# Kernel tuning notes

Measured on AMD Instinct MI355X. Metric: run time of the kernel, lower is better.

## Reference

```python
import jax, jax.numpy as jnp
from jax import lax
import numpy as np

B, C, H, W = 1, 128, 32, 32
OC, K = 128, 3
STRIDE, PAD, DIL = 1, 1, 1
ARRAY_SIZE = 32
QUANT = 8


def setup_inputs() -> dict:
    key = jax.random.key(0)
    k1, k2, k3 = jax.random.split(key, 3)
    x = jax.random.normal(k1, (B, C, H, W), dtype=jnp.float32)
    weight = jax.random.normal(k2, (OC, C, K, K), dtype=jnp.float32) * 0.05
    bias = jax.random.normal(k3, (OC,), dtype=jnp.float32) * 0.05
    return {"x": x, "weight": weight, "bias": bias}


def _conv(x, w, b):
    out = lax.conv_general_dilated(
        x, w, window_strides=(STRIDE, STRIDE),
        padding=((PAD, PAD), (PAD, PAD)),
        rhs_dilation=(DIL, DIL),
        dimension_numbers=("NCHW", "OIHW", "NCHW"))
    return out + b[None, :, None, None]


def _unfold(x, oh, ow):
    # torch F.unfold: (B, C*K*K, L) with channel-major ordering (c, kh, kw)
    xp = jnp.pad(x, ((0, 0), (0, 0), (PAD, PAD), (PAD, PAD)))
    cols = jnp.stack(
        [xp[:, :, i:i + oh, j:j + ow] for i in range(K) for j in range(K)],
        axis=2)  # (B, C, K*K, OH, OW)
    return cols.reshape(B, C * K * K, oh * ow)


def reference(x, weight, bias):
    oh = (H + 2 * PAD - DIL * (K - 1) - 1) // STRIDE + 1
    ow = (W + 2 * PAD - DIL * (K - 1) - 1) // STRIDE + 1
    L = oh * ow
    qmax = float(2 ** QUANT - 1)

    # --- set_quant_params: per-spatial-location scale/zero_point from full conv out ---
    out_full = _conv(x, weight, bias).reshape(1, OC, -1)  # (1, OC, L)
    mx = jnp.max(out_full, axis=1)  # (1, L)
    mn = jnp.min(out_full, axis=1)
    scale = (mx - mn) / qmax
    zp = jnp.clip(-mn / scale, 0.0, qmax)
    zp = jnp.where(jnp.isnan(zp), 0.0, zp)
    zp = jnp.trunc(zp)  # .int() truncation
    scale = lax.stop_gradient(scale)[:, None, None, :]  # (1,1,1,L)
    zp = lax.stop_gradient(zp)[:, None, None, :]

    # --- unfold + explicit elementwise multiply (crossbar expansion) ---
    cols = _unfold(x, oh, ow)                       # (B, C*K*K, L)
    pre = cols[:, None, :, :] * weight.reshape(1, OC, C * K * K, 1)  # (B,OC,CKK,L)

    # pad front of dim 2 to a multiple of array_size (pads a full chunk if divisible)
    ckk = C * K * K
    pad_d3 = ARRAY_SIZE - ckk % ARRAY_SIZE
    pre = jnp.pad(pre, ((0, 0), (0, 0), (pad_d3, 0), (0, 0)))

    # block-sum over array_size chunks (crossbar partial sums)
    n_chunks = (ckk + pad_d3) // ARRAY_SIZE
    accu = pre.reshape(B, OC, n_chunks, ARRAY_SIZE, L).sum(axis=3)  # (B,OC,n_chunks,L)

    # per-chunk fake-quant (Quant8F) with straight-through estimator
    q = jnp.clip(jnp.round(accu / scale) + zp, 0.0, qmax)
    deq = (q - zp) * scale
    quant_accu = accu + lax.stop_gradient(deq - accu)

    # reduce over chunks -> conv output (note: bias is NOT added in original forward)
    return quant_accu.sum(axis=2).reshape(B, OC, oh, ow)
```

## Files before the change

kernel.cpp:

```cpp
#include <hip/hip_runtime.h>

#define L_     1024
#define CKK_   1152
#define QMAX_  255.0f
#define NCH    36
#define PSTR_  (131072 + 64)

__global__ __launch_bounds__(256) void gemm_chunks(
    const float* __restrict__ x,
    const float* __restrict__ w,
    float* __restrict__ planes)
{
    __shared__ __align__(16) float Wb[32][132];
    __shared__ __align__(16) float xs[32][64];

    const int t   = threadIdx.x;
    const int l0  = blockIdx.x * 64;
    const int j   = blockIdx.y;
    const int d0  = j * 32;
    const int oh0 = l0 >> 5;

    float4 wld[4];
    int    wo[4], wk[4];
#pragma unroll
    for (int it = 0; it < 4; it++) {
        const int f4 = it * 256 + t;
        wo[it]  = f4 >> 3;
        wk[it]  = (f4 & 7) * 4;
        wld[it] = *(const float4*)(w + wo[it] * CKK_ + d0 + wk[it]);
    }

    float xl[8];
    int   xk[8], xll[8];
#pragma unroll
    for (int it = 0; it < 8; it++) {
        const int e  = it * 256 + t;
        const int k  = e >> 6, ll = e & 63;
        const int d  = d0 + k;
        const int c  = d / 9, r = d - 9 * c;
        const int kh = r / 3, kw = r - 3 * kh;
        const int iy = oh0 + (ll >> 5) + kh - 1;
        const int ix = (ll & 31) + kw - 1;
        const bool ok = ((unsigned)iy < 32u) & ((unsigned)ix < 32u);
        const int idx = ok ? (c * 1024 + iy * 32 + ix) : 0;
        const float v = x[idx];
        xl[it] = ok ? v : 0.f;
        xk[it] = k; xll[it] = ll;
    }

#pragma unroll
    for (int it = 0; it < 4; it++) {
        Wb[wk[it] + 0][wo[it]] = wld[it].x;
        Wb[wk[it] + 1][wo[it]] = wld[it].y;
        Wb[wk[it] + 2][wo[it]] = wld[it].z;
        Wb[wk[it] + 3][wo[it]] = wld[it].w;
    }
#pragma unroll
    for (int it = 0; it < 8; it++)
        xs[xk[it]][xll[it]] = xl[it];
    __syncthreads();

    const int oc0 = (t & 31) * 4;
    const int ll0 = (t >> 5) * 8;
    float acc[4][8];
#pragma unroll
    for (int r = 0; r < 4; r++)
#pragma unroll
        for (int i = 0; i < 8; i++) acc[r][i] = 0.f;

#pragma unroll
    for (int k = 0; k < 32; k++) {
        const float4 wv = *(const float4*)&Wb[k][oc0];
        const float4 xa = *(const float4*)&xs[k][ll0];
        const float4 xb = *(const float4*)&xs[k][ll0 + 4];
        acc[0][0] = fmaf(wv.x, xa.x, acc[0][0]);
        acc[0][1] = fmaf(wv.x, xa.y, acc[0][1]);
        acc[0][2] = fmaf(wv.x, xa.z, acc[0][2]);
        acc[0][3] = fmaf(wv.x, xa.w, acc[0][3]);
        acc[0][4] = fmaf(wv.x, xb.x, acc[0][4]);
        acc[0][5] = fmaf(wv.x, xb.y, acc[0][5]);
        acc[0][6] = fmaf(wv.x, xb.z, acc[0][6]);
        acc[0][7] = fmaf(wv.x, xb.w, acc[0][7]);
        acc[1][0] = fmaf(wv.y, xa.x, acc[1][0]);
        acc[1][1] = fmaf(wv.y, xa.y, acc[1][1]);
        acc[1][2] = fmaf(wv.y, xa.z, acc[1][2]);
        acc[1][3] = fmaf(wv.y, xa.w, acc[1][3]);
        acc[1][4] = fmaf(wv.y, xb.x, acc[1][4]);
        acc[1][5] = fmaf(wv.y, xb.y, acc[1][5]);
        acc[1][6] = fmaf(wv.y, xb.z, acc[1][6]);
        acc[1][7] = fmaf(wv.y, xb.w, acc[1][7]);
        acc[2][0] = fmaf(wv.z, xa.x, acc[2][0]);
        acc[2][1] = fmaf(wv.z, xa.y, acc[2][1]);
        acc[2][2] = fmaf(wv.z, xa.z, acc[2][2]);
        acc[2][3] = fmaf(wv.z, xa.w, acc[2][3]);
        acc[2][4] = fmaf(wv.z, xb.x, acc[2][4]);
        acc[2][5] = fmaf(wv.z, xb.y, acc[2][5]);
        acc[2][6] = fmaf(wv.z, xb.z, acc[2][6]);
        acc[2][7] = fmaf(wv.z, xb.w, acc[2][7]);
        acc[3][0] = fmaf(wv.w, xa.x, acc[3][0]);
        acc[3][1] = fmaf(wv.w, xa.y, acc[3][1]);
        acc[3][2] = fmaf(wv.w, xa.z, acc[3][2]);
        acc[3][3] = fmaf(wv.w, xa.w, acc[3][3]);
        acc[3][4] = fmaf(wv.w, xb.x, acc[3][4]);
        acc[3][5] = fmaf(wv.w, xb.y, acc[3][5]);
        acc[3][6] = fmaf(wv.w, xb.z, acc[3][6]);
        acc[3][7] = fmaf(wv.w, xb.w, acc[3][7]);
    }

    float* dst = planes + (size_t)j * PSTR_ + (size_t)l0 * 128;
#pragma unroll
    for (int i = 0; i < 8; i++)
        *(float4*)(dst + (ll0 + i) * 128 + oc0) =
            make_float4(acc[0][i], acc[1][i], acc[2][i], acc[3][i]);
}

__global__ __launch_bounds__(256) void fused_mq(
    const float* __restrict__ planes,
    const float* __restrict__ bias,
    float* __restrict__ out)
{
    __shared__ float part[256];
    __shared__ float mnb[128], mxb[128];
    __shared__ float s_sc, s_zp, s_iv;
    const int t  = threadIdx.x;
    const int oc = t & 127, jh = t >> 7;
    const int l  = blockIdx.x;

    const float* p = planes + (size_t)(jh * 18) * PSTR_ + (size_t)l * 128 + oc;
    float v[18];
#pragma unroll
    for (int j = 0; j < 18; j++) v[j] = p[(size_t)j * PSTR_];

    float s = 0.f;
#pragma unroll
    for (int j = 0; j < 18; j++) s += v[j];
    part[t] = s;
    __syncthreads();

    if (t < 128) {
        const float tot = part[t] + part[t + 128] + bias[t];
        mnb[t] = tot;
        mxb[t] = tot;
    }
    __syncthreads();
#pragma unroll
    for (int st = 64; st > 0; st >>= 1) {
        if (t < st) {
            mnb[t] = fminf(mnb[t], mnb[t + st]);
            mxb[t] = fmaxf(mxb[t], mxb[t + st]);
        }
        __syncthreads();
    }
    if (t == 0) {
        const float amn = mnb[0], amx = mxb[0];
        const float sv  = (amx - amn) / QMAX_;
        float z = -amn / sv;
        z = fmaxf(z, 0.f);
        z = fminf(z, QMAX_);
        z = truncf(z);
        s_sc = sv;
        s_zp = z;
        s_iv = 1.0f / sv;
    }
    __syncthreads();

    const float sc = s_sc, zv = s_zp, iv = s_iv;
    float q = 0.f;
#pragma unroll
    for (int j = 0; j < 18; j++) {
        float qn = rintf(v[j] * iv) + zv;
        qn = fminf(fmaxf(qn, 0.f), QMAX_);
        q += (qn - zv) * sc;
    }
    part[t] = q;
    __syncthreads();

    if (t < 128)
        out[oc * L_ + l] = part[t] + part[t + 128];
}

template <bool QUANT>
__global__ __launch_bounds__(256) void cas_direct(
    const float* __restrict__ x, const float* __restrict__ w,
    float* __restrict__ out, const float* __restrict__ scale,
    const float* __restrict__ zp, const float* __restrict__ inv)
{
    const int t = threadIdx.x;
    const int ocBase = blockIdx.x * 16;
    const int l = blockIdx.y * 256 + t;
    const int oh = l >> 5, ow = l & 31;

    float sc = 0.f, zv = 0.f, iv = 0.f;
    if (QUANT) { sc = scale[l]; zv = zp[l]; iv = inv[l]; }

    float acc[16];
#pragma unroll
    for (int oc = 0; oc < 16; oc++) acc[oc] = 0.f;

    for (int j = 0; j < NCH; j++) {
        const int d0 = j * 32;
        float xv[32];
#pragma unroll
        for (int dd = 0; dd < 32; dd++) {
            const int d = d0 + dd, c = d / 9, r = d - 9 * c;
            const int kh = r / 3, kw = r - 3 * kh;
            const int off = c * 1024 + (kh - 1) * 32 + (kw - 1);
            const bool ok = ((unsigned)(oh + kh - 1) < 32u) &
                            ((unsigned)(ow + kw - 1) < 32u);
            const int idx = ok ? (off + l) : 0;
            const float vv = x[idx];
            xv[dd] = ok ? vv : 0.f;
        }
#pragma unroll
        for (int oc = 0; oc < 16; oc++) {
            const float4* wp = (const float4*)(w + (ocBase + oc) * CKK_ + d0);
            float pa = 0.f, pb = 0.f;
#pragma unroll
            for (int k4 = 0; k4 < 8; k4++) {
                const float4 wv = wp[k4];
                float& pr = (k4 < 4) ? pa : pb;
                pr = fmaf(wv.x, xv[4 * k4 + 0], pr);
                pr = fmaf(wv.y, xv[4 * k4 + 1], pr);
                pr = fmaf(wv.z, xv[4 * k4 + 2], pr);
                pr = fmaf(wv.w, xv[4 * k4 + 3], pr);
            }
            const float s2 = pa + pb;
            if (QUANT) {
                float qn = rintf(s2 * iv) + zv;
                qn = fminf(fmaxf(qn, 0.f), QMAX_);
                acc[oc] += (qn - zv) * sc;
            } else {
                acc[oc] += s2;
            }
        }
    }
#pragma unroll
    for (int oc = 0; oc < 16; oc++)
        out[(ocBase + oc) * L_ + l] = acc[oc];
}

__global__ __launch_bounds__(256) void minmax_conv(
    const float* __restrict__ conv, const float* __restrict__ bias,
    float* __restrict__ scale, float* __restrict__ zp, float* __restrict__ inv)
{
    __shared__ float smn[16][17], smx[16][17];
    const int t = threadIdx.x, li = t & 15, g = t >> 4;
    const int l = blockIdx.x * 16 + li;
    float mn = INFINITY, mx = -INFINITY;
#pragma unroll
    for (int i = 0; i < 8; i++) {
        const int oc = g * 8 + i;
        const float v = conv[oc * L_ + l] + bias[oc];
        mn = fminf(mn, v); mx = fmaxf(mx, v);
    }
    smn[g][li] = mn; smx[g][li] = mx;
    __syncthreads();
    if (t < 16) {
        const int l2 = blockIdx.x * 16 + t;
        float amn = smn[0][t], amx = smx[0][t];
#pragma unroll
        for (int g2 = 1; g2 < 16; g2++) {
            amn = fminf(amn, smn[g2][t]); amx = fmaxf(amx, smx[g2][t]);
        }
        const float s = (amx - amn) / QMAX_;
        float z = -amn / s;
        z = fminf(fmaxf(z, 0.f), QMAX_);
        z = truncf(z);
        scale[l2] = s; zp[l2] = z; inv[l2] = 1.0f / s;
    }
}

extern "C" void kernel_launch(void* const* d_in, const int* in_sizes, int n_in,
                              void* d_out, int out_size, void* d_ws, size_t ws_size,
                              hipStream_t stream) {
    const float* x    = (const float*)d_in[0];
    const float* w    = (const float*)d_in[1];
    const float* bias = (const float*)d_in[2];
    float* out = (float*)d_out;
    float* ws  = (float*)d_ws;

    const size_t main_need = (size_t)NCH * PSTR_ * 4;
    if (ws_size >= main_need) {
        float* planes = ws;
        gemm_chunks<<<dim3(16, NCH), 256, 0, stream>>>(x, w, planes);
        fused_mq<<<1024, 256, 0, stream>>>(planes, bias, out);
    } else {
        float* conv  = ws;
        float* scale = conv + 131072;
        float* zpv   = scale + 1024;
        float* inv   = zpv + 1024;
        cas_direct<false><<<dim3(8, 4), 256, 0, stream>>>(x, w, conv, nullptr, nullptr, nullptr);
        minmax_conv<<<64, 256, 0, stream>>>(conv, bias, scale, zpv, inv);
        cas_direct<true><<<dim3(8, 4), 256, 0, stream>>>(x, w, out, scale, zpv, inv);
    }
}
```

Measured before the change: 74.77 us.

## Split fused min-max/quant kernel into two passes with tiled transposed output store

The single fused kernel, which held all 36 chunk partials per location in registers and wrote the output with a stride of L, is split in two. The first kernel computes per-location scale, zero point and inverse into workspace, visiting locations in a swizzled order. The second kernel re-reads the partial planes and quantises them, staging results through a shared-memory 16x16 tile so the output writes are coalesced. The cost is a second full read of the 36 planes and one extra kernel launch, in exchange for removing the strided scattered output writes.

```diff
diff --git a/kernel.cpp b/kernel.cpp
--- a/kernel.cpp
+++ b/kernel.cpp
@@ -114,26 +114,23 @@
             make_float4(acc[0][i], acc[1][i], acc[2][i], acc[3][i]);
 }
 
-__global__ __launch_bounds__(256) void fused_mq(
+__global__ __launch_bounds__(256) void minmax_k(
     const float* __restrict__ planes,
     const float* __restrict__ bias,
-    float* __restrict__ out)
+    float* __restrict__ scale, float* __restrict__ zp, float* __restrict__ inv)
 {
     __shared__ float part[256];
     __shared__ float mnb[128], mxb[128];
-    __shared__ float s_sc, s_zp, s_iv;
     const int t  = threadIdx.x;
     const int oc = t & 127, jh = t >> 7;
-    const int l  = blockIdx.x;
+    const int b  = blockIdx.x;
+    const int xx = b & 7, rr = b >> 3;
+    const int l  = (xx + 8 * (rr & 7)) * 16 + (rr >> 3);
 
     const float* p = planes + (size_t)(jh * 18) * PSTR_ + (size_t)l * 128 + oc;
-    float v[18];
-#pragma unroll
-    for (int j = 0; j < 18; j++) v[j] = p[(size_t)j * PSTR_];
-
     float s = 0.f;
 #pragma unroll
-    for (int j = 0; j < 18; j++) s += v[j];
+    for (int j = 0; j < 18; j++) s += p[(size_t)j * PSTR_];
     part[t] = s;
     __syncthreads();
 
@@ -158,25 +155,43 @@
         z = fmaxf(z, 0.f);
         z = fminf(z, QMAX_);
         z = truncf(z);
-        s_sc = sv;
-        s_zp = z;
-        s_iv = 1.0f / sv;
-    }
-    __syncthreads();
-
-    const float sc = s_sc, zv = s_zp, iv = s_iv;
-    float q = 0.f;
-#pragma unroll
-    for (int j = 0; j < 18; j++) {
-        float qn = rintf(v[j] * iv) + zv;
-        qn = fminf(fmaxf(qn, 0.f), QMAX_);
-        q += (qn - zv) * sc;
-    }
-    part[t] = q;
-    __syncthreads();
-
-    if (t < 128)
-        out[oc * L_ + l] = part[t] + part[t + 128];
+        scale[l] = sv;
+        zp[l]    = z;
+        inv[l]   = 1.0f / sv;
+    }
+}
+
+__global__ __launch_bounds__(256) void quant_k(
+    const float* __restrict__ planes,
+    const float* __restrict__ scale, const float* __restrict__ zp,
+    const float* __restrict__ inv, float* __restrict__ out)
+{
+    __shared__ float otile[16][17];
+    const int t   = threadIdx.x;
+    const int oi  = t & 15, li = t >> 4;
+    const int ocg = blockIdx.x & 7, lg = blockIdx.x >> 3;
+    const int oc  = ocg * 16 + oi, l = lg * 16 + li;
+
+    const float sv = scale[l], zv = zp[l], iv = inv[l];
+    const float* p = planes + (size_t)l * 128 + oc;
+
+    float qa = 0.f, qb = 0.f;
+#pragma unroll
+    for (int j = 0; j < NCH; j += 2) {
+        const float a0 = p[(size_t)j * PSTR_];
+        const float a1 = p[(size_t)(j + 1) * PSTR_];
+        float q0 = rintf(a0 * iv) + zv;
+        q0 = fminf(fmaxf(q0, 0.f), QMAX_);
+        qa += (q0 - zv) * sv;
+        float q1 = rintf(a1 * iv) + zv;
+        q1 = fminf(fmaxf(q1, 0.f), QMAX_);
+        qb += (q1 - zv) * sv;
+    }
+    otile[oi][li] = qa + qb;
+    __syncthreads();
+
+    const int ocs = t >> 4, ls = t & 15;
+    out[(ocg * 16 + ocs) * L_ + lg * 16 + ls] = otile[ocs][ls];
 }
 
 template <bool QUANT>
@@ -279,11 +294,16 @@
     float* out = (float*)d_out;
     float* ws  = (float*)d_ws;
 
-    const size_t main_need = (size_t)NCH * PSTR_ * 4;
+    const size_t main_need = ((size_t)NCH * PSTR_ + 3 * 1024) * 4;
     if (ws_size >= main_need) {
         float* planes = ws;
+        float* scale  = planes + (size_t)NCH * PSTR_;
+        float* zpv    = scale + 1024;
+        float* inv    = zpv + 1024;
+
         gemm_chunks<<<dim3(16, NCH), 256, 0, stream>>>(x, w, planes);
-        fused_mq<<<1024, 256, 0, stream>>>(planes, bias, out);
+        minmax_k<<<1024, 256, 0, stream>>>(planes, bias, scale, zpv, inv);
+        quant_k<<<512, 256, 0, stream>>>(planes, scale, zpv, inv, out);
     } else {
         float* conv  = ws;
         float* scale = conv + 131072;
```

New measurement: 79.38 us. 1.06x slower.
